# Optimization experiments

Measured on AMD Instinct MI355X. Metric: run time of the kernel, lower is better.

## Reference

```python
import jax, jax.numpy as jnp
import numpy as np

B, N, IN, HD, NH, L, OUT = 256, 128, 9, 128, 8, 4, 60
DH = HD // NH
ALPHA = 0.6
EPS = 1e-5

def _ln(x, g, b):
    m = jnp.mean(x, axis=-1, keepdims=True)
    v = jnp.mean((x - m) ** 2, axis=-1, keepdims=True)
    return (x - m) * jax.lax.rsqrt(v + EPS) * g + b

def setup_inputs():
    key = jax.random.key(0)
    ks = jax.random.split(key, 30)
    p = lambda i, s: jax.random.normal(ks[i], s, jnp.float32) * 0.02
    strong = (jax.random.uniform(ks[25], (N, N)) < 0.15).astype(jnp.float32)
    strong = jnp.maximum(strong, jnp.eye(N, dtype=jnp.float32))  # self loops
    weak_mask = (jax.random.uniform(ks[26], (N, N)) < 0.10).astype(jnp.float32)
    return {
        'x': jax.random.normal(ks[0], (B, N, IN), jnp.float32),
        'conv_w': p(1, (HD, IN)), 'conv_b': p(2, (HD,)),
        'bn_gamma': jnp.ones((HD,), jnp.float32), 'bn_beta': jnp.zeros((HD,), jnp.float32),
        'bn_mean': jnp.zeros((HD,), jnp.float32), 'bn_var': jnp.ones((HD,), jnp.float32),
        'W': p(3, (L, HD, HD)), 'a_src': p(4, (L, NH, DH)), 'a_dst': p(5, (L, NH, DH)),
        'ln_g': jnp.ones((L, HD), jnp.float32), 'ln_b': jnp.zeros((L, HD), jnp.float32),
        'ffn_w1': p(6, (L, HD, 2 * HD)), 'ffn_b1': p(7, (L, 2 * HD)),
        'ffn_w2': p(8, (L, 2 * HD, HD)), 'ffn_b2': p(9, (L, HD)),
        'norm_g': jnp.ones((HD,), jnp.float32), 'norm_b': jnp.zeros((HD,), jnp.float32),
        'proj_w': p(10, (HD, HD)), 'proj_b': p(11, (HD,)),
        'head_w1': p(12, (HD, HD // 2)), 'head_b1': p(13, (HD // 2,)),
        'head_w2': p(14, (HD // 2, OUT)), 'head_b2': p(15, (OUT,)),
        'strong_adj': strong, 'weak_mask': weak_mask,
        'weak_param': p(16, (N, N)), 'edge_weight_adj': p(17, (N, N)),
    }

def reference(x, conv_w, conv_b, bn_gamma, bn_beta, bn_mean, bn_var, W, a_src, a_dst, ln_g, ln_b, ffn_w1, ffn_b1, ffn_w2, ffn_b2, norm_g, norm_b, proj_w, proj_b, head_w1, head_b1, head_w2, head_b2, strong_adj, weak_mask, weak_param, edge_weight_adj):
    # embedding: Conv1d(k=1) == per-node linear, then eval-mode BatchNorm1d + ReLU
    h = jnp.einsum('bni,oi->bno', x, conv_w) + conv_b  # [B,N,HD]
    h = (h - bn_mean) * jax.lax.rsqrt(bn_var + EPS) * bn_gamma + bn_beta
    h = jax.nn.relu(h)
    # weak adjacency: learnable gated edges, row-normalized (shared across layers)
    Aw = jax.nn.sigmoid(weak_param) * weak_mask
    Aw = Aw / (jnp.sum(Aw, axis=-1, keepdims=True) + EPS)  # [N,N]
    for i in range(L):
        res = h
        hp = jnp.einsum('bnd,de->bne', h, W[i]).reshape(B, N, NH, DH)
        s = jnp.einsum('bnhd,hd->bnh', hp, a_src[i])
        t = jnp.einsum('bnhd,hd->bnh', hp, a_dst[i])
        e = jax.nn.leaky_relu(s[:, :, None, :] + t[:, None, :, :], 0.2)  # [B,N,N,H]
        e = e + edge_weight_adj[None, :, :, None]  # learned per-edge bias
        e = jnp.where(strong_adj[None, :, :, None] > 0, e, jnp.float32(-1e9))
        att = jax.nn.softmax(e, axis=2)  # softmax over neighbors j
        strong_out = jnp.einsum('bijh,bjhd->bihd', att, hp)
        weak_out = jnp.einsum('ij,bjhd->bihd', Aw, hp)
        g = jax.nn.relu(ALPHA * strong_out + (1.0 - ALPHA) * weak_out).reshape(B, N, HD)
        g = _ln(g, ln_g[i], ln_b[i])
        g = jax.nn.relu(g @ ffn_w1[i] + ffn_b1[i]) @ ffn_w2[i] + ffn_b2[i]
        h = g + res
    h = _ln(h, norm_g, norm_b)
    h = h @ proj_w + proj_b
    h = jnp.mean(h, axis=1)  # mean-pool over nodes -> [B,HD]
    h = jax.nn.relu(h @ head_w1 + head_b1)
    return h @ head_w2 + head_b2  # [B,OUT]
```

## Files before the change

kernel.cpp:

```cpp
#include <hip/hip_runtime.h>
#include <hip/hip_bf16.h>

typedef __hip_bfloat16 bf16;
typedef unsigned short u16;
typedef __attribute__((ext_vector_type(8))) short bfrag;
typedef __attribute__((ext_vector_type(4))) float cfrag;

union BF { bfrag v; u16 u[8]; unsigned w[4]; };
union CF { cfrag v; float f[4]; };

#define MFMA(a,b,c) __builtin_amdgcn_mfma_f32_16x16x32_bf16(a,b,c,0,0,0)

#define BB   256
#define NN   128
#define IND  9
#define HDD  128
#define LLY  4
#define OUTD 60
#define LOG2E 1.44269504f
#define STR  136

__device__ __forceinline__ float b2f(bf16 v){ return __bfloat162float(v); }
__device__ __forceinline__ float u2f(u16 u){ return __uint_as_float(((unsigned)u) << 16); }
__device__ __forceinline__ u16 f2bf_bits(float f){
    unsigned u = __float_as_uint(f);
    return (u16)((u + 0x7FFFu + ((u >> 16) & 1u)) >> 16);
}
__device__ __forceinline__ unsigned pk2(float a, float b){
    union { __hip_bfloat162 h; unsigned u; } c;
    c.h = __float22bfloat162_rn(make_float2(a, b));
    return c.u;
}
__device__ __forceinline__ float wave_sum(float v){
    #pragma unroll
    for (int m = 32; m; m >>= 1) v += __shfl_xor(v, m, 64);
    return v;
}
__device__ __forceinline__ float ldin(const void* p, int i, bool isbf){
    return isbf ? b2f(((const bf16*)p)[i]) : ((const float*)p)[i];
}

struct SrcPtrs { const void* p[28]; };

__device__ const int NCV_OFF[19] = {0,1152,1280,1408,1536,1664,1792,2304,2816,3840,
                                    4352,4480,4608,20992,21120,29312,29376,33216,33276};
__device__ const int NCV_SRC[18] = {1,2,3,4,5,6,10,11,13,15,16,17,18,19,20,21,22,23};

__global__ __launch_bounds__(256) void k_prep(
    SrcPtrs S, float* __restrict__ pf,
    u16* __restrict__ WT, u16* __restrict__ w1T, u16* __restrict__ w2T,
    u16* __restrict__ WAb, u16* __restrict__ ew2, u16* __restrict__ Aw16,
    int* __restrict__ flagOut)
{
    const unsigned* xw = (const unsigned*)S.p[0];
    int lane = threadIdx.x & 63;
    int cnt = 0;
    for (int i = lane; i < 512; i += 64) {
        float v = __uint_as_float((xw[i] & 0xFFFFu) << 16);
        if (!(fabsf(v) < 32.f)) cnt++;
    }
    bool isbf = wave_sum((float)cnt) < 16.f;
    if (blockIdx.x == 0 && threadIdx.x == 0) *flagOut = isbf ? 1 : 0;

    int blk = blockIdx.x, tid = threadIdx.x;
    if (blk < 131) {
        int idx = blk * 256 + tid;
        if (idx < 33276) {
            int y = 17;
            #pragma unroll 1
            for (int t = 1; t < 18; t++) if (idx < NCV_OFF[t]) { y = t - 1; break; }
            pf[idx] = ldin(S.p[NCV_SRC[y]], idx - NCV_OFF[y], isbf);
        }
    } else if (blk < 387) {
        int j = (blk - 131) * 256 + tid;
        int l = j >> 14, r = j & 16383, n = r >> 7, k = r & 127;
        WT[j] = f2bf_bits(ldin(S.p[7], (l << 14) + k * 128 + n, isbf));
    } else if (blk < 899) {
        int j = (blk - 387) * 256 + tid;
        int l = j >> 15, r = j & 32767, n = r >> 7, k = r & 127;
        w1T[j] = f2bf_bits(ldin(S.p[12], (l << 15) + k * 256 + n, isbf));
    } else if (blk < 1411) {
        int j = (blk - 899) * 256 + tid;
        int l = j >> 15, r = j & 32767, n = r >> 8, k = r & 255;
        w2T[j] = f2bf_bits(ldin(S.p[14], (l << 15) + k * 128 + n, isbf));
    } else if (blk < 1443) {
        int j = (blk - 1411) * 256 + tid;
        int l = j >> 11, r = j & 2047, n = r >> 7, k = r & 127;
        int h = n & 7;
        const void* ap = (n < 8) ? S.p[8] : S.p[9];
        float sacc = 0.f;
        #pragma unroll 1
        for (int d = 0; d < 16; d++)
            sacc += ldin(S.p[7], l * 16384 + k * 128 + h * 16 + d, isbf)
                  * ldin(ap, l * 128 + h * 16 + d, isbf);
        WAb[j] = f2bf_bits(sacc);
    } else if (blk < 1507) {
        int j = (blk - 1443) * 256 + tid;
        float sav = ldin(S.p[24], j, isbf);
        float ewv = ldin(S.p[27], j, isbf);
        ew2[j] = f2bf_bits(sav > 0.f ? ewv * LOG2E : -1e30f);
    } else {
        __shared__ float red[2];
        int i = blk - 1507, j = tid & 127;
        float v = 0.f;
        if (tid < 128) {
            float wmv = ldin(S.p[25], i * 128 + j, isbf);
            float wpv = ldin(S.p[26], i * 128 + j, isbf);
            v = wmv / (1.f + __expf(-wpv));
            float sm = wave_sum(v);
            if ((tid & 63) == 0) red[tid >> 6] = sm;
        }
        __syncthreads();
        if (tid < 128) {
            float tot = red[0] + red[1];
            Aw16[i * 128 + j] = f2bf_bits(v / (tot + 1e-5f));
        }
    }
}

#define LDSB (2*128*STR*2 + 8192)
__global__ __launch_bounds__(512, 2) void k_net(
    const void* __restrict__ xraw, const int* __restrict__ flag,
    const float* __restrict__ pf,
    const u16* __restrict__ WTg, const u16* __restrict__ WAbg,
    const u16* __restrict__ Awg, const u16* __restrict__ ew2g,
    const u16* __restrict__ w1Tg, const u16* __restrict__ w2Tg,
    void* __restrict__ outv)
{
    extern __shared__ __align__(16) char smem[];
    u16* Abuf = (u16*)smem;
    u16* Bbuf = Abuf + 128 * STR;
    float* st2 = (float*)(Bbuf + 128 * STR);
    float* s2  = st2;
    u16*   t2u = (u16*)(st2 + 1024);

    const int b = blockIdx.x;
    const int tid = threadIdx.x, lane = tid & 63, wv = tid >> 6;
    const int l15 = lane & 15, kg = lane >> 4;
    const int wrow = wv * 16;
    const bool isbf = (*flag != 0);

    float hreg[8][4];

    {
        float xr[4][9];
        #pragma unroll
        for (int r = 0; r < 4; r++) {
            int bn = b * NN + wrow + kg * 4 + r;
            #pragma unroll
            for (int k = 0; k < IND; k++) xr[r][k] = ldin(xraw, bn * IND + k, isbf);
        }
        #pragma unroll 1
        for (int nt = 0; nt < 8; nt++) {
            int d = nt * 16 + l15;
            float cwreg[IND];
            #pragma unroll
            for (int k = 0; k < IND; k++) cwreg[k] = pf[d * IND + k];
            float scale = rsqrtf(pf[1664 + d] + 1e-5f) * pf[1280 + d];
            float bias  = pf[1408 + d] - pf[1536 + d] * scale;
            float cbd   = pf[1152 + d];
            #pragma unroll
            for (int r = 0; r < 4; r++) {
                float a = cbd;
                #pragma unroll
                for (int k = 0; k < IND; k++) a = fmaf(xr[r][k], cwreg[k], a);
                a = fmaxf(fmaf(a, scale, bias), 0.f);
                hreg[nt][r] = a;
                Abuf[(wrow + kg * 4 + r) * STR + d] = f2bf_bits(a);
            }
        }
    }

    const int arow = wrow + l15;

    #pragma unroll 1
    for (int l = 0; l < LLY; l++) {
        const u16* WT  = WTg  + l * 16384;
        const u16* WAb = WAbg + l * 2048;
        const u16* w1T = w1Tg + l * 32768;
        const u16* w2T = w2Tg + l * 32768;
        const float* fb1 = pf + 2816 + l * 256;
        const float* fb2 = pf + 3840 + l * 128;
        const float* lng = pf + 1792 + l * 128;
        const float* lnb = pf + 2304 + l * 128;

        __syncthreads();

        {
            CF acc[8], ast;
            #pragma unroll
            for (int r = 0; r < 4; r++) ast.f[r] = 0.f;
            #pragma unroll
            for (int nt = 0; nt < 8; nt++)
                #pragma unroll
                for (int r = 0; r < 4; r++) acc[nt].f[r] = 0.f;
            #pragma unroll 1
            for (int kk = 0; kk < 4; kk++) {
                bfrag af  = *(const bfrag*)&Abuf[arow * STR + kk*32 + kg*8];
                bfrag wab = *(const bfrag*)&WAb[l15 * 128 + kk*32 + kg*8];
                ast.v = MFMA(af, wab, ast.v);
                #pragma unroll
                for (int nt = 0; nt < 8; nt++) {
                    bfrag bw = *(const bfrag*)&WT[(nt*16 + l15) * 128 + kk*32 + kg*8];
                    acc[nt].v = MFMA(af, bw, acc[nt].v);
                }
            }
            #pragma unroll
            for (int nt = 0; nt < 8; nt++) {
                int col = nt*16 + l15;
                #pragma unroll
                for (int rp = 0; rp < 2; rp++) {
                    int row = wrow + kg*4 + rp*2;
                    *(unsigned*)&Bbuf[col * STR + row] = pk2(acc[nt].f[rp*2], acc[nt].f[rp*2+1]);
                }
            }
            #pragma unroll
            for (int r = 0; r < 4; r++) {
                int node = wrow + kg*4 + r;
                float v = ast.f[r] * LOG2E;
                if (l15 < 8) s2[l15 * 128 + node] = v;
                else         t2u[(l15 - 8) * 128 + node] = f2bf_bits(v);
            }
        }
        __syncthreads();

        CF accW[8];
        #pragma unroll
        for (int nt = 0; nt < 8; nt++)
            #pragma unroll
            for (int r = 0; r < 4; r++) accW[nt].f[r] = 0.f;
        #pragma unroll 1
        for (int kk = 0; kk < 4; kk++) {
            bfrag awf = *(const bfrag*)&Awg[arow * 128 + kk*32 + kg*8];
            #pragma unroll
            for (int nt = 0; nt < 8; nt++) {
                bfrag hb2 = *(const bfrag*)&Bbuf[(nt*16 + l15) * STR + kk*32 + kg*8];
                accW[nt].v = MFMA(awf, hb2, accW[nt].v);
            }
        }

        CF accS[8];
        #pragma unroll
        for (int nt = 0; nt < 8; nt++)
            #pragma unroll
            for (int r = 0; r < 4; r++) accS[nt].f[r] = 0.f;
        #pragma unroll 1
        for (int h = 0; h < 8; h++) {
            bfrag hb[4];
            #pragma unroll
            for (int kk = 0; kk < 4; kk++)
                hb[kk] = *(const bfrag*)&Bbuf[(h*16 + l15) * STR + kk*32 + kg*8];
            float sA = s2[h * 128 + arow];
            float pv[4][8];
            float sm = 0.f;
            #pragma unroll
            for (int kk = 0; kk < 4; kk++) {
                BF tb; tb.v = *(const bfrag*)&t2u[h * 128 + kk*32 + kg*8];
                BF e2; e2.v = *(const bfrag*)&ew2g[arow * 128 + kk*32 + kg*8];
                #pragma unroll
                for (int j = 0; j < 8; j++) {
                    float x2 = sA + u2f(tb.u[j]);
                    float lk = fmaxf(x2, 0.2f * x2);
                    float p = __builtin_amdgcn_exp2f(lk + u2f(e2.u[j]));
                    pv[kk][j] = p; sm += p;
                }
            }
            sm += __shfl_xor(sm, 16, 64);
            sm += __shfl_xor(sm, 32, 64);
            float inv = __builtin_amdgcn_rcpf(sm);
            #pragma unroll
            for (int kk = 0; kk < 4; kk++) {
                BF pb;
                #pragma unroll
                for (int q = 0; q < 4; q++)
                    pb.w[q] = pk2(pv[kk][2*q] * inv, pv[kk][2*q+1] * inv);
                accS[h].v = MFMA(pb.v, hb[kk], accS[h].v);
            }
        }
        __syncthreads();

        {
            float gv[8][4];
            #pragma unroll
            for (int nt = 0; nt < 8; nt++)
                #pragma unroll
                for (int r = 0; r < 4; r++)
                    gv[nt][r] = fmaxf(0.6f * accS[nt].f[r] + 0.4f * accW[nt].f[r], 0.f);
            #pragma unroll
            for (int r = 0; r < 4; r++) {
                float s1 = 0.f, sq = 0.f;
                #pragma unroll
                for (int nt = 0; nt < 8; nt++) { float x = gv[nt][r]; s1 += x; sq = fmaf(x, x, sq); }
                #pragma unroll
                for (int m = 1; m <= 8; m <<= 1) { s1 += __shfl_xor(s1, m, 64); sq += __shfl_xor(sq, m, 64); }
                float mu = s1 * (1.f / 128.f);
                float var = sq * (1.f / 128.f) - mu * mu;
                float rs = rsqrtf(fmaxf(var, 0.f) + 1e-5f);
                #pragma unroll
                for (int nt = 0; nt < 8; nt++) {
                    int col = nt*16 + l15;
                    Bbuf[(wrow + kg*4 + r) * STR + col] =
                        f2bf_bits(fmaf((gv[nt][r] - mu) * rs, lng[col], lnb[col]));
                }
            }
        }

        CF acc2[8];
        #pragma unroll
        for (int nt = 0; nt < 8; nt++)
            #pragma unroll
            for (int r = 0; r < 4; r++) acc2[nt].f[r] = 0.f;
        #pragma unroll 1
        for (int nh = 0; nh < 2; nh++) {
            CF a1[8];
            #pragma unroll
            for (int nt = 0; nt < 8; nt++)
                #pragma unroll
                for (int r = 0; r < 4; r++) a1[nt].f[r] = 0.f;
            #pragma unroll 1
            for (int kk = 0; kk < 4; kk++) {
                bfrag gf = *(const bfrag*)&Bbuf[arow * STR + kk*32 + kg*8];
                #pragma unroll
                for (int nt = 0; nt < 8; nt++) {
                    bfrag wf = *(const bfrag*)&w1T[(nh*128 + nt*16 + l15) * 128 + kk*32 + kg*8];
                    a1[nt].v = MFMA(gf, wf, a1[nt].v);
                }
            }
            #pragma unroll
            for (int nt = 0; nt < 8; nt++) {
                int col = nt*16 + l15;
                float b1v = fb1[nh*128 + col];
                #pragma unroll
                for (int r = 0; r < 4; r++)
                    Abuf[(wrow + kg*4 + r) * STR + col] = f2bf_bits(fmaxf(a1[nt].f[r] + b1v, 0.f));
            }
            #pragma unroll 1
            for (int kk = 0; kk < 4; kk++) {
                bfrag hf = *(const bfrag*)&Abuf[arow * STR + kk*32 + kg*8];
                #pragma unroll
                for (int nt = 0; nt < 8; nt++) {
                    bfrag wf = *(const bfrag*)&w2T[(nt*16 + l15) * 256 + nh*128 + kk*32 + kg*8];
                    acc2[nt].v = MFMA(hf, wf, acc2[nt].v);
                }
            }
        }

        #pragma unroll
        for (int nt = 0; nt < 8; nt++) {
            float b2v = fb2[nt*16 + l15];
            #pragma unroll
            for (int r = 0; r < 4; r++) hreg[nt][r] += acc2[nt].f[r] + b2v;
        }
        if (l < LLY - 1) {
            #pragma unroll
            for (int nt = 0; nt < 8; nt++) {
                int col = nt*16 + l15;
                #pragma unroll
                for (int r = 0; r < 4; r++)
                    Abuf[(wrow + kg*4 + r) * STR + col] = f2bf_bits(hreg[nt][r]);
            }
        }
    }

    const float* ng = pf + 4352;
    const float* nb = pf + 4480;
    float pacc[8];
    #pragma unroll
    for (int nt = 0; nt < 8; nt++) pacc[nt] = 0.f;
    #pragma unroll
    for (int r = 0; r < 4; r++) {
        float s1 = 0.f, sq = 0.f;
        #pragma unroll
        for (int nt = 0; nt < 8; nt++) { float x = hreg[nt][r]; s1 += x; sq = fmaf(x, x, sq); }
        #pragma unroll
        for (int m = 1; m <= 8; m <<= 1) { s1 += __shfl_xor(s1, m, 64); sq += __shfl_xor(sq, m, 64); }
        float mu = s1 * (1.f / 128.f);
        float var = sq * (1.f / 128.f) - mu * mu;
        float rs = rsqrtf(fmaxf(var, 0.f) + 1e-5f);
        #pragma unroll
        for (int nt = 0; nt < 8; nt++) {
            int col = nt*16 + l15;
            pacc[nt] += fmaf((hreg[nt][r] - mu) * rs, ng[col], nb[col]);
        }
    }
    #pragma unroll
    for (int nt = 0; nt < 8; nt++) {
        pacc[nt] += __shfl_xor(pacc[nt], 16, 64);
        pacc[nt] += __shfl_xor(pacc[nt], 32, 64);
    }
    __syncthreads();
    if (kg == 0) {
        #pragma unroll
        for (int nt = 0; nt < 8; nt++) st2[wv * 128 + nt*16 + l15] = pacc[nt];
    }
    __syncthreads();
    if (tid < 128) {
        float tot = 0.f;
        #pragma unroll
        for (int w = 0; w < 8; w++) tot += st2[w * 128 + tid];
        st2[1024 + tid] = tot * (1.f / 128.f);
    }
    __syncthreads();
    {
        int e = tid & 127, kq = tid >> 7;
        float a = 0.f;
        #pragma unroll 4
        for (int k = kq * 32; k < kq * 32 + 32; k++)
            a = fmaf(st2[1024 + k], pf[4608 + k * 128 + e], a);
        st2[1152 + kq * 128 + e] = a;
    }
    __syncthreads();
    if (tid < 128)
        st2[1664 + tid] = st2[1152 + tid] + st2[1280 + tid] + st2[1408 + tid] + st2[1536 + tid]
                        + pf[20992 + tid];
    __syncthreads();
    if (tid < 64) {
        float a1 = pf[29312 + tid];
        #pragma unroll 4
        for (int k = 0; k < 128; k++) a1 = fmaf(st2[1664 + k], pf[21120 + k * 64 + tid], a1);
        st2[1792 + tid] = fmaxf(a1, 0.f);
    }
    __syncthreads();
    if (tid < OUTD) {
        float a2 = pf[33216 + tid];
        #pragma unroll 4
        for (int k = 0; k < 64; k++) a2 = fmaf(st2[1792 + k], pf[29376 + k * OUTD + tid], a2);
        if (isbf) ((bf16*)outv)[b * OUTD + tid] = __float2bfloat16(a2);
        else      ((float*)outv)[b * OUTD + tid] = a2;
    }
}

extern "C" void kernel_launch(void* const* d_in, const int* in_sizes, int n_in,
                              void* d_out, int out_size, void* d_ws, size_t ws_size,
                              hipStream_t stream)
{
    float* ws = (float*)d_ws;
    float* pf = ws;
    int*   flag = (int*)(ws + 33280);
    u16* WT16   = (u16*)(ws + 33536);
    u16* w1T16  = WT16 + 65536;
    u16* w2T16  = w1T16 + 131072;
    u16* WAb16  = w2T16 + 131072;
    u16* Aw16   = WAb16 + 8192;
    u16* ew2p   = Aw16 + 16384;

    SrcPtrs S;
    for (int i = 0; i < 28; i++) S.p[i] = d_in[i];

    hipFuncSetAttribute((const void*)k_net,
                        hipFuncAttributeMaxDynamicSharedMemorySize, LDSB);

    k_prep<<<1635, 256, 0, stream>>>(S, pf, WT16, w1T16, w2T16, WAb16, ew2p, Aw16, flag);
    k_net<<<BB, 512, LDSB, stream>>>(d_in[0], flag, pf,
                                     WT16, WAb16, Aw16, ew2p, w1T16, w2T16, d_out);
}
```

Before: 353.0 us.

## Split each node-row tile across two waves by column halves with 1024-thread blocks

Doubles the block to 1024 threads so each 16-row strip is handled by two waves, each owning half the 128 feature columns (and half the attention heads). LayerNorm statistics are combined across the two halves through a small LDS stat buffer. A third LDS buffer holds the FFN hidden layer and the h/feature buffers ping-pong across layers. The aim is more waves per block to hide latency and halve per-thread register pressure, at the cost of more LDS and extra barriers.

```diff
diff --git a/kernel.cpp b/kernel.cpp
--- a/kernel.cpp
+++ b/kernel.cpp
@@ -118,8 +118,8 @@
     }
 }
 
-#define LDSB (2*128*STR*2 + 8192)
-__global__ __launch_bounds__(512, 2) void k_net(
+#define LDSB (3*128*STR*2 + 8192)
+__global__ __launch_bounds__(1024, 4) void k_net(
     const void* __restrict__ xraw, const int* __restrict__ flag,
     const float* __restrict__ pf,
     const u16* __restrict__ WTg, const u16* __restrict__ WAbg,
@@ -130,17 +130,21 @@
     extern __shared__ __align__(16) char smem[];
     u16* Abuf = (u16*)smem;
     u16* Bbuf = Abuf + 128 * STR;
-    float* st2 = (float*)(Bbuf + 128 * STR);
+    u16* Cbuf = Bbuf + 128 * STR;
+    float* st2 = (float*)(Cbuf + 128 * STR);
     float* s2  = st2;
     u16*   t2u = (u16*)(st2 + 1024);
+    float* stat = st2 + 1536;
 
     const int b = blockIdx.x;
     const int tid = threadIdx.x, lane = tid & 63, wv = tid >> 6;
     const int l15 = lane & 15, kg = lane >> 4;
-    const int wrow = wv * 16;
+    const int wpair = wv & 7, half = wv >> 3;
+    const int wrow = wpair * 16;
+    const int colbase = half * 64;
     const bool isbf = (*flag != 0);
 
-    float hreg[8][4];
+    float hreg[4][4];
 
     {
         float xr[4][9];
@@ -151,8 +155,8 @@
             for (int k = 0; k < IND; k++) xr[r][k] = ldin(xraw, bn * IND + k, isbf);
         }
         #pragma unroll 1
-        for (int nt = 0; nt < 8; nt++) {
-            int d = nt * 16 + l15;
+        for (int nt = 0; nt < 4; nt++) {
+            int d = colbase + nt * 16 + l15;
             float cwreg[IND];
             #pragma unroll
             for (int k = 0; k < IND; k++) cwreg[k] = pf[d * IND + k];
@@ -172,6 +176,8 @@
     }
 
     const int arow = wrow + l15;
+    u16* hA = Abuf;
+    u16* hB = Bbuf;
 
     #pragma unroll 1
     for (int l = 0; l < LLY; l++) {
@@ -187,211 +193,248 @@
         __syncthreads();
 
         {
-            CF acc[8], ast;
+            CF acc[4], ast;
             #pragma unroll
             for (int r = 0; r < 4; r++) ast.f[r] = 0.f;
             #pragma unroll
-            for (int nt = 0; nt < 8; nt++)
+            for (int nt = 0; nt < 4; nt++)
                 #pragma unroll
                 for (int r = 0; r < 4; r++) acc[nt].f[r] = 0.f;
             #pragma unroll 1
             for (int kk = 0; kk < 4; kk++) {
-                bfrag af  = *(const bfrag*)&Abuf[arow * STR + kk*32 + kg*8];
-                bfrag wab = *(const bfrag*)&WAb[l15 * 128 + kk*32 + kg*8];
-                ast.v = MFMA(af, wab, ast.v);
-                #pragma unroll
-                for (int nt = 0; nt < 8; nt++) {
-                    bfrag bw = *(const bfrag*)&WT[(nt*16 + l15) * 128 + kk*32 + kg*8];
+                bfrag af = *(const bfrag*)&hA[arow * STR + kk*32 + kg*8];
+                if (half == 0) {
+                    bfrag wab = *(const bfrag*)&WAb[l15 * 128 + kk*32 + kg*8];
+                    ast.v = MFMA(af, wab, ast.v);
+                }
+                #pragma unroll
+                for (int nt = 0; nt < 4; nt++) {
+                    bfrag bw = *(const bfrag*)&WT[(colbase + nt*16 + l15) * 128 + kk*32 + kg*8];
                     acc[nt].v = MFMA(af, bw, acc[nt].v);
                 }
             }
             #pragma unroll
-            for (int nt = 0; nt < 8; nt++) {
-                int col = nt*16 + l15;
+            for (int nt = 0; nt < 4; nt++) {
+                int col = colbase + nt*16 + l15;
                 #pragma unroll
                 for (int rp = 0; rp < 2; rp++) {
                     int row = wrow + kg*4 + rp*2;
-                    *(unsigned*)&Bbuf[col * STR + row] = pk2(acc[nt].f[rp*2], acc[nt].f[rp*2+1]);
-                }
-            }
-            #pragma unroll
-            for (int r = 0; r < 4; r++) {
-                int node = wrow + kg*4 + r;
-                float v = ast.f[r] * LOG2E;
-                if (l15 < 8) s2[l15 * 128 + node] = v;
-                else         t2u[(l15 - 8) * 128 + node] = f2bf_bits(v);
-            }
-        }
-        __syncthreads();
-
-        CF accW[8];
-        #pragma unroll
-        for (int nt = 0; nt < 8; nt++)
+                    *(unsigned*)&hB[col * STR + row] = pk2(acc[nt].f[rp*2], acc[nt].f[rp*2+1]);
+                }
+            }
+            if (half == 0) {
+                #pragma unroll
+                for (int r = 0; r < 4; r++) {
+                    int node = wrow + kg*4 + r;
+                    float v = ast.f[r] * LOG2E;
+                    if (l15 < 8) s2[l15 * 128 + node] = v;
+                    else         t2u[(l15 - 8) * 128 + node] = f2bf_bits(v);
+                }
+            }
+        }
+        __syncthreads();
+
+        CF accS[4];
+        #pragma unroll
+        for (int nt = 0; nt < 4; nt++)
+            #pragma unroll
+            for (int r = 0; r < 4; r++) accS[nt].f[r] = 0.f;
+        {
+            BF e2r[4];
+            #pragma unroll
+            for (int kk = 0; kk < 4; kk++)
+                e2r[kk].v = *(const bfrag*)&ew2g[arow * 128 + kk*32 + kg*8];
+            #pragma unroll 1
+            for (int hi = 0; hi < 4; hi++) {
+                int h = half * 4 + hi;
+                bfrag hb[4];
+                #pragma unroll
+                for (int kk = 0; kk < 4; kk++)
+                    hb[kk] = *(const bfrag*)&hB[(h*16 + l15) * STR + kk*32 + kg*8];
+                float sA = s2[h * 128 + arow];
+                float pv[4][8];
+                float sm = 0.f;
+                #pragma unroll
+                for (int kk = 0; kk < 4; kk++) {
+                    BF tb; tb.v = *(const bfrag*)&t2u[h * 128 + kk*32 + kg*8];
+                    #pragma unroll
+                    for (int j = 0; j < 8; j++) {
+                        float x2 = sA + u2f(tb.u[j]);
+                        float lk = fmaxf(x2, 0.2f * x2);
+                        float p = __builtin_amdgcn_exp2f(lk + u2f(e2r[kk].u[j]));
+                        pv[kk][j] = p; sm += p;
+                    }
+                }
+                sm += __shfl_xor(sm, 16, 64);
+                sm += __shfl_xor(sm, 32, 64);
+                float inv = __builtin_amdgcn_rcpf(sm);
+                #pragma unroll
+                for (int kk = 0; kk < 4; kk++) {
+                    BF pb;
+                    #pragma unroll
+                    for (int q = 0; q < 4; q++)
+                        pb.w[q] = pk2(pv[kk][2*q] * inv, pv[kk][2*q+1] * inv);
+                    accS[hi].v = MFMA(pb.v, hb[kk], accS[hi].v);
+                }
+            }
+        }
+
+        CF accW[4];
+        #pragma unroll
+        for (int nt = 0; nt < 4; nt++)
             #pragma unroll
             for (int r = 0; r < 4; r++) accW[nt].f[r] = 0.f;
         #pragma unroll 1
         for (int kk = 0; kk < 4; kk++) {
             bfrag awf = *(const bfrag*)&Awg[arow * 128 + kk*32 + kg*8];
             #pragma unroll
-            for (int nt = 0; nt < 8; nt++) {
-                bfrag hb2 = *(const bfrag*)&Bbuf[(nt*16 + l15) * STR + kk*32 + kg*8];
+            for (int nt = 0; nt < 4; nt++) {
+                bfrag hb2 = *(const bfrag*)&hB[(colbase + nt*16 + l15) * STR + kk*32 + kg*8];
                 accW[nt].v = MFMA(awf, hb2, accW[nt].v);
             }
         }
-
-        CF accS[8];
-        #pragma unroll
-        for (int nt = 0; nt < 8; nt++)
-            #pragma unroll
-            for (int r = 0; r < 4; r++) accS[nt].f[r] = 0.f;
-        #pragma unroll 1
-        for (int h = 0; h < 8; h++) {
-            bfrag hb[4];
-            #pragma unroll
-            for (int kk = 0; kk < 4; kk++)
-                hb[kk] = *(const bfrag*)&Bbuf[(h*16 + l15) * STR + kk*32 + kg*8];
-            float sA = s2[h * 128 + arow];
-            float pv[4][8];
-            float sm = 0.f;
-            #pragma unroll
-            for (int kk = 0; kk < 4; kk++) {
-                BF tb; tb.v = *(const bfrag*)&t2u[h * 128 + kk*32 + kg*8];
-                BF e2; e2.v = *(const bfrag*)&ew2g[arow * 128 + kk*32 + kg*8];
-                #pragma unroll
-                for (int j = 0; j < 8; j++) {
-                    float x2 = sA + u2f(tb.u[j]);
-                    float lk = fmaxf(x2, 0.2f * x2);
-                    float p = __builtin_amdgcn_exp2f(lk + u2f(e2.u[j]));
-                    pv[kk][j] = p; sm += p;
-                }
-            }
-            sm += __shfl_xor(sm, 16, 64);
-            sm += __shfl_xor(sm, 32, 64);
-            float inv = __builtin_amdgcn_rcpf(sm);
-            #pragma unroll
-            for (int kk = 0; kk < 4; kk++) {
-                BF pb;
-                #pragma unroll
-                for (int q = 0; q < 4; q++)
-                    pb.w[q] = pk2(pv[kk][2*q] * inv, pv[kk][2*q+1] * inv);
-                accS[h].v = MFMA(pb.v, hb[kk], accS[h].v);
-            }
-        }
-        __syncthreads();
-
-        {
-            float gv[8][4];
-            #pragma unroll
-            for (int nt = 0; nt < 8; nt++)
-                #pragma unroll
-                for (int r = 0; r < 4; r++)
-                    gv[nt][r] = fmaxf(0.6f * accS[nt].f[r] + 0.4f * accW[nt].f[r], 0.f);
-            #pragma unroll
-            for (int r = 0; r < 4; r++) {
-                float s1 = 0.f, sq = 0.f;
-                #pragma unroll
-                for (int nt = 0; nt < 8; nt++) { float x = gv[nt][r]; s1 += x; sq = fmaf(x, x, sq); }
-                #pragma unroll
-                for (int m = 1; m <= 8; m <<= 1) { s1 += __shfl_xor(s1, m, 64); sq += __shfl_xor(sq, m, 64); }
-                float mu = s1 * (1.f / 128.f);
-                float var = sq * (1.f / 128.f) - mu * mu;
-                float rs = rsqrtf(fmaxf(var, 0.f) + 1e-5f);
-                #pragma unroll
-                for (int nt = 0; nt < 8; nt++) {
-                    int col = nt*16 + l15;
-                    Bbuf[(wrow + kg*4 + r) * STR + col] =
-                        f2bf_bits(fmaf((gv[nt][r] - mu) * rs, lng[col], lnb[col]));
-                }
-            }
-        }
-
-        CF acc2[8];
-        #pragma unroll
-        for (int nt = 0; nt < 8; nt++)
-            #pragma unroll
-            for (int r = 0; r < 4; r++) acc2[nt].f[r] = 0.f;
+        __syncthreads();
+
+        float gv[4][4];
+        #pragma unroll
+        for (int nt = 0; nt < 4; nt++)
+            #pragma unroll
+            for (int r = 0; r < 4; r++)
+                gv[nt][r] = fmaxf(0.6f * accS[nt].f[r] + 0.4f * accW[nt].f[r], 0.f);
+        #pragma unroll
+        for (int r = 0; r < 4; r++) {
+            float s1 = 0.f, sq = 0.f;
+            #pragma unroll
+            for (int nt = 0; nt < 4; nt++) { float x = gv[nt][r]; s1 += x; sq = fmaf(x, x, sq); }
+            #pragma unroll
+            for (int m = 1; m <= 8; m <<= 1) { s1 += __shfl_xor(s1, m, 64); sq += __shfl_xor(sq, m, 64); }
+            if (l15 == 0) {
+                int row = wrow + kg*4 + r;
+                stat[(half * 128 + row) * 2]     = s1;
+                stat[(half * 128 + row) * 2 + 1] = sq;
+            }
+        }
+        __syncthreads();
+        #pragma unroll
+        for (int r = 0; r < 4; r++) {
+            int row = wrow + kg*4 + r;
+            float s1t = stat[row * 2]     + stat[(128 + row) * 2];
+            float sqt = stat[row * 2 + 1] + stat[(128 + row) * 2 + 1];
+            float mu = s1t * (1.f / 128.f);
+            float var = sqt * (1.f / 128.f) - mu * mu;
+            float rs = rsqrtf(fmaxf(var, 0.f) + 1e-5f);
+            #pragma unroll
+            for (int nt = 0; nt < 4; nt++) {
+                int col = colbase + nt*16 + l15;
+                hB[row * STR + col] = f2bf_bits(fmaf((gv[nt][r] - mu) * rs, lng[col], lnb[col]));
+            }
+        }
+        __syncthreads();
+
         #pragma unroll 1
         for (int nh = 0; nh < 2; nh++) {
-            CF a1[8];
-            #pragma unroll
-            for (int nt = 0; nt < 8; nt++)
+            u16* hid = nh ? Cbuf : hA;
+            CF a1[4];
+            #pragma unroll
+            for (int nt = 0; nt < 4; nt++)
                 #pragma unroll
                 for (int r = 0; r < 4; r++) a1[nt].f[r] = 0.f;
             #pragma unroll 1
             for (int kk = 0; kk < 4; kk++) {
-                bfrag gf = *(const bfrag*)&Bbuf[arow * STR + kk*32 + kg*8];
-                #pragma unroll
-                for (int nt = 0; nt < 8; nt++) {
-                    bfrag wf = *(const bfrag*)&w1T[(nh*128 + nt*16 + l15) * 128 + kk*32 + kg*8];
+                bfrag gf = *(const bfrag*)&hB[arow * STR + kk*32 + kg*8];
+                #pragma unroll
+                for (int nt = 0; nt < 4; nt++) {
+                    bfrag wf = *(const bfrag*)&w1T[(nh*128 + colbase + nt*16 + l15) * 128 + kk*32 + kg*8];
                     a1[nt].v = MFMA(gf, wf, a1[nt].v);
                 }
             }
             #pragma unroll
-            for (int nt = 0; nt < 8; nt++) {
-                int col = nt*16 + l15;
-                float b1v = fb1[nh*128 + col];
+            for (int nt = 0; nt < 4; nt++) {
+                int lcol = colbase + nt*16 + l15;
+                float b1v = fb1[nh*128 + lcol];
                 #pragma unroll
                 for (int r = 0; r < 4; r++)
-                    Abuf[(wrow + kg*4 + r) * STR + col] = f2bf_bits(fmaxf(a1[nt].f[r] + b1v, 0.f));
-            }
-            #pragma unroll 1
-            for (int kk = 0; kk < 4; kk++) {
-                bfrag hf = *(const bfrag*)&Abuf[arow * STR + kk*32 + kg*8];
-                #pragma unroll
-                for (int nt = 0; nt < 8; nt++) {
-                    bfrag wf = *(const bfrag*)&w2T[(nt*16 + l15) * 256 + nh*128 + kk*32 + kg*8];
-                    acc2[nt].v = MFMA(hf, wf, acc2[nt].v);
-                }
-            }
-        }
-
-        #pragma unroll
-        for (int nt = 0; nt < 8; nt++) {
-            float b2v = fb2[nt*16 + l15];
+                    hid[(wrow + kg*4 + r) * STR + lcol] = f2bf_bits(fmaxf(a1[nt].f[r] + b1v, 0.f));
+            }
+        }
+        __syncthreads();
+
+        CF acc2[4];
+        #pragma unroll
+        for (int nt = 0; nt < 4; nt++)
+            #pragma unroll
+            for (int r = 0; r < 4; r++) acc2[nt].f[r] = 0.f;
+        #pragma unroll 1
+        for (int kk = 0; kk < 8; kk++) {
+            const u16* hid = (kk < 4) ? hA : Cbuf;
+            bfrag hf = *(const bfrag*)&hid[arow * STR + (kk & 3)*32 + kg*8];
+            #pragma unroll
+            for (int nt = 0; nt < 4; nt++) {
+                bfrag wf = *(const bfrag*)&w2T[(colbase + nt*16 + l15) * 256 + kk*32 + kg*8];
+                acc2[nt].v = MFMA(hf, wf, acc2[nt].v);
+            }
+        }
+
+        #pragma unroll
+        for (int nt = 0; nt < 4; nt++) {
+            float b2v = fb2[colbase + nt*16 + l15];
             #pragma unroll
             for (int r = 0; r < 4; r++) hreg[nt][r] += acc2[nt].f[r] + b2v;
         }
         if (l < LLY - 1) {
             #pragma unroll
-            for (int nt = 0; nt < 8; nt++) {
-                int col = nt*16 + l15;
+            for (int nt = 0; nt < 4; nt++) {
+                int col = colbase + nt*16 + l15;
                 #pragma unroll
                 for (int r = 0; r < 4; r++)
-                    Abuf[(wrow + kg*4 + r) * STR + col] = f2bf_bits(hreg[nt][r]);
-            }
-        }
+                    hB[(wrow + kg*4 + r) * STR + col] = f2bf_bits(hreg[nt][r]);
+            }
+        }
+        { u16* t = hA; hA = hB; hB = t; }
     }
 
     const float* ng = pf + 4352;
     const float* nb = pf + 4480;
-    float pacc[8];
-    #pragma unroll
-    for (int nt = 0; nt < 8; nt++) pacc[nt] = 0.f;
     #pragma unroll
     for (int r = 0; r < 4; r++) {
         float s1 = 0.f, sq = 0.f;
         #pragma unroll
-        for (int nt = 0; nt < 8; nt++) { float x = hreg[nt][r]; s1 += x; sq = fmaf(x, x, sq); }
+        for (int nt = 0; nt < 4; nt++) { float x = hreg[nt][r]; s1 += x; sq = fmaf(x, x, sq); }
         #pragma unroll
         for (int m = 1; m <= 8; m <<= 1) { s1 += __shfl_xor(s1, m, 64); sq += __shfl_xor(sq, m, 64); }
-        float mu = s1 * (1.f / 128.f);
-        float var = sq * (1.f / 128.f) - mu * mu;
+        if (l15 == 0) {
+            int row = wrow + kg*4 + r;
+            stat[(half * 128 + row) * 2]     = s1;
+            stat[(half * 128 + row) * 2 + 1] = sq;
+        }
+    }
+    __syncthreads();
+    float pacc[4];
+    #pragma unroll
+    for (int nt = 0; nt < 4; nt++) pacc[nt] = 0.f;
+    #pragma unroll
+    for (int r = 0; r < 4; r++) {
+        int row = wrow + kg*4 + r;
+        float s1t = stat[row * 2]     + stat[(128 + row) * 2];
+        float sqt = stat[row * 2 + 1] + stat[(128 + row) * 2 + 1];
+        float mu = s1t * (1.f / 128.f);
+        float var = sqt * (1.f / 128.f) - mu * mu;
         float rs = rsqrtf(fmaxf(var, 0.f) + 1e-5f);
         #pragma unroll
-        for (int nt = 0; nt < 8; nt++) {
-            int col = nt*16 + l15;
+        for (int nt = 0; nt < 4; nt++) {
+            int col = colbase + nt*16 + l15;
             pacc[nt] += fmaf((hreg[nt][r] - mu) * rs, ng[col], nb[col]);
         }
     }
     #pragma unroll
-    for (int nt = 0; nt < 8; nt++) {
+    for (int nt = 0; nt < 4; nt++) {
         pacc[nt] += __shfl_xor(pacc[nt], 16, 64);
         pacc[nt] += __shfl_xor(pacc[nt], 32, 64);
     }
-    __syncthreads();
     if (kg == 0) {
         #pragma unroll
-        for (int nt = 0; nt < 8; nt++) st2[wv * 128 + nt*16 + l15] = pacc[nt];
+        for (int nt = 0; nt < 4; nt++)
+            st2[wpair * 128 + colbase + nt*16 + l15] = pacc[nt];
     }
     __syncthreads();
     if (tid < 128) {
@@ -401,7 +444,7 @@
         st2[1024 + tid] = tot * (1.f / 128.f);
     }
     __syncthreads();
-    {
+    if (tid < 512) {
         int e = tid & 127, kq = tid >> 7;
         float a = 0.f;
         #pragma unroll 4
@@ -451,6 +494,6 @@
                         hipFuncAttributeMaxDynamicSharedMemorySize, LDSB);
 
     k_prep<<<1635, 256, 0, stream>>>(S, pf, WT16, w1T16, w2T16, WAb16, ew2p, Aw16, flag);
-    k_net<<<BB, 512, LDSB, stream>>>(d_in[0], flag, pf,
-                                     WT16, WAb16, Aw16, ew2p, w1T16, w2T16, d_out);
-}
+    k_net<<<BB, 1024, LDSB, stream>>>(d_in[0], flag, pf,
+                                      WT16, WAb16, Aw16, ew2p, w1T16, w2T16, d_out);
+}
```

Measured after the change: 382.5 us. +8.4%, slower.

## Defer softmax normalization, packed-float edge math, hoist edge bias, unroll MFMA loops

Applied to the files above, without the earlier changes.

The attention softmax now feeds unnormalized exponentials straight into the MFMA and rescales the 16x16 accumulator afterwards with a per-row reciprocal fetched by shuffle. This removes the per-element multiply and the register buffering of all 32 probabilities per head. The per-edge bias is decoded once per layer instead of once per head, and the leaky-relu/add math uses 2-wide float vectors so packed instructions can be used. Bf16 conversions switch to the hardware packed convert, and several MFMA k-loops are unrolled by two, which may raise register pressure.

```diff
diff --git a/kernel.cpp b/kernel.cpp
--- a/kernel.cpp
+++ b/kernel.cpp
@@ -5,6 +5,7 @@
 typedef unsigned short u16;
 typedef __attribute__((ext_vector_type(8))) short bfrag;
 typedef __attribute__((ext_vector_type(4))) float cfrag;
+typedef __attribute__((ext_vector_type(2))) float f32x2;
 
 union BF { bfrag v; u16 u[8]; unsigned w[4]; };
 union CF { cfrag v; float f[4]; };
@@ -30,6 +31,9 @@
     union { __hip_bfloat162 h; unsigned u; } c;
     c.h = __float22bfloat162_rn(make_float2(a, b));
     return c.u;
+}
+__device__ __forceinline__ u16 f2bf1(float f){
+    return (u16)pk2(f, 0.f);
 }
 __device__ __forceinline__ float wave_sum(float v){
     #pragma unroll
@@ -166,7 +170,7 @@
                 for (int k = 0; k < IND; k++) a = fmaf(xr[r][k], cwreg[k], a);
                 a = fmaxf(fmaf(a, scale, bias), 0.f);
                 hreg[nt][r] = a;
-                Abuf[(wrow + kg * 4 + r) * STR + d] = f2bf_bits(a);
+                Abuf[(wrow + kg * 4 + r) * STR + d] = f2bf1(a);
             }
         }
     }
@@ -194,7 +198,7 @@
             for (int nt = 0; nt < 8; nt++)
                 #pragma unroll
                 for (int r = 0; r < 4; r++) acc[nt].f[r] = 0.f;
-            #pragma unroll 1
+            #pragma unroll 2
             for (int kk = 0; kk < 4; kk++) {
                 bfrag af  = *(const bfrag*)&Abuf[arow * STR + kk*32 + kg*8];
                 bfrag wab = *(const bfrag*)&WAb[l15 * 128 + kk*32 + kg*8];
@@ -219,62 +223,77 @@
                 int node = wrow + kg*4 + r;
                 float v = ast.f[r] * LOG2E;
                 if (l15 < 8) s2[l15 * 128 + node] = v;
-                else         t2u[(l15 - 8) * 128 + node] = f2bf_bits(v);
+                else         t2u[(l15 - 8) * 128 + node] = f2bf1(v);
             }
         }
         __syncthreads();
 
+        CF accS[8];
+        #pragma unroll
+        for (int nt = 0; nt < 8; nt++)
+            #pragma unroll
+            for (int r = 0; r < 4; r++) accS[nt].f[r] = 0.f;
+        {
+            f32x2 e2f[4][4];
+            #pragma unroll
+            for (int kk = 0; kk < 4; kk++) {
+                BF e2; e2.v = *(const bfrag*)&ew2g[arow * 128 + kk*32 + kg*8];
+                #pragma unroll
+                for (int q = 0; q < 4; q++) {
+                    unsigned w = e2.w[q];
+                    e2f[kk][q].x = __uint_as_float(w << 16);
+                    e2f[kk][q].y = __uint_as_float(w & 0xffff0000u);
+                }
+            }
+            #pragma unroll 1
+            for (int h = 0; h < 8; h++) {
+                float sA = s2[h * 128 + arow];
+                f32x2 sA2; sA2.x = sA; sA2.y = sA;
+                float sm = 0.f;
+                #pragma unroll
+                for (int kk = 0; kk < 4; kk++) {
+                    bfrag hb = *(const bfrag*)&Bbuf[(h*16 + l15) * STR + kk*32 + kg*8];
+                    BF tb; tb.v = *(const bfrag*)&t2u[h * 128 + kk*32 + kg*8];
+                    BF pb;
+                    #pragma unroll
+                    for (int q = 0; q < 4; q++) {
+                        unsigned w = tb.w[q];
+                        f32x2 tv;
+                        tv.x = __uint_as_float(w << 16);
+                        tv.y = __uint_as_float(w & 0xffff0000u);
+                        f32x2 x2 = sA2 + tv;
+                        f32x2 lk = __builtin_elementwise_max(x2, x2 * 0.2f);
+                        f32x2 ex = lk + e2f[kk][q];
+                        float p0 = __builtin_amdgcn_exp2f(ex.x);
+                        float p1 = __builtin_amdgcn_exp2f(ex.y);
+                        sm += p0 + p1;
+                        pb.w[q] = pk2(p0, p1);
+                    }
+                    accS[h].v = MFMA(pb.v, hb, accS[h].v);
+                }
+                sm += __shfl_xor(sm, 16, 64);
+                sm += __shfl_xor(sm, 32, 64);
+                float inv = __builtin_amdgcn_rcpf(sm);
+                #pragma unroll
+                for (int r = 0; r < 4; r++) {
+                    float invr = __shfl(inv, kg * 4 + r, 64);
+                    accS[h].f[r] *= invr;
+                }
+            }
+        }
+
         CF accW[8];
         #pragma unroll
         for (int nt = 0; nt < 8; nt++)
             #pragma unroll
             for (int r = 0; r < 4; r++) accW[nt].f[r] = 0.f;
-        #pragma unroll 1
+        #pragma unroll 2
         for (int kk = 0; kk < 4; kk++) {
             bfrag awf = *(const bfrag*)&Awg[arow * 128 + kk*32 + kg*8];
             #pragma unroll
             for (int nt = 0; nt < 8; nt++) {
                 bfrag hb2 = *(const bfrag*)&Bbuf[(nt*16 + l15) * STR + kk*32 + kg*8];
                 accW[nt].v = MFMA(awf, hb2, accW[nt].v);
-            }
-        }
-
-        CF accS[8];
-        #pragma unroll
-        for (int nt = 0; nt < 8; nt++)
-            #pragma unroll
-            for (int r = 0; r < 4; r++) accS[nt].f[r] = 0.f;
-        #pragma unroll 1
-        for (int h = 0; h < 8; h++) {
-            bfrag hb[4];
-            #pragma unroll
-            for (int kk = 0; kk < 4; kk++)
-                hb[kk] = *(const bfrag*)&Bbuf[(h*16 + l15) * STR + kk*32 + kg*8];
-            float sA = s2[h * 128 + arow];
-            float pv[4][8];
-            float sm = 0.f;
-            #pragma unroll
-            for (int kk = 0; kk < 4; kk++) {
-                BF tb; tb.v = *(const bfrag*)&t2u[h * 128 + kk*32 + kg*8];
-                BF e2; e2.v = *(const bfrag*)&ew2g[arow * 128 + kk*32 + kg*8];
-                #pragma unroll
-                for (int j = 0; j < 8; j++) {
-                    float x2 = sA + u2f(tb.u[j]);
-                    float lk = fmaxf(x2, 0.2f * x2);
-                    float p = __builtin_amdgcn_exp2f(lk + u2f(e2.u[j]));
-                    pv[kk][j] = p; sm += p;
-                }
-            }
-            sm += __shfl_xor(sm, 16, 64);
-            sm += __shfl_xor(sm, 32, 64);
-            float inv = __builtin_amdgcn_rcpf(sm);
-            #pragma unroll
-            for (int kk = 0; kk < 4; kk++) {
-                BF pb;
-                #pragma unroll
-                for (int q = 0; q < 4; q++)
-                    pb.w[q] = pk2(pv[kk][2*q] * inv, pv[kk][2*q+1] * inv);
-                accS[h].v = MFMA(pb.v, hb[kk], accS[h].v);
             }
         }
         __syncthreads();
@@ -300,7 +319,7 @@
                 for (int nt = 0; nt < 8; nt++) {
                     int col = nt*16 + l15;
                     Bbuf[(wrow + kg*4 + r) * STR + col] =
-                        f2bf_bits(fmaf((gv[nt][r] - mu) * rs, lng[col], lnb[col]));
+                        f2bf1(fmaf((gv[nt][r] - mu) * rs, lng[col], lnb[col]));
                 }
             }
         }
@@ -317,7 +336,7 @@
             for (int nt = 0; nt < 8; nt++)
                 #pragma unroll
                 for (int r = 0; r < 4; r++) a1[nt].f[r] = 0.f;
-            #pragma unroll 1
+            #pragma unroll 2
             for (int kk = 0; kk < 4; kk++) {
                 bfrag gf = *(const bfrag*)&Bbuf[arow * STR + kk*32 + kg*8];
                 #pragma unroll
@@ -332,9 +351,9 @@
                 float b1v = fb1[nh*128 + col];
                 #pragma unroll
                 for (int r = 0; r < 4; r++)
-                    Abuf[(wrow + kg*4 + r) * STR + col] = f2bf_bits(fmaxf(a1[nt].f[r] + b1v, 0.f));
-            }
-            #pragma unroll 1
+                    Abuf[(wrow + kg*4 + r) * STR + col] = f2bf1(fmaxf(a1[nt].f[r] + b1v, 0.f));
+            }
+            #pragma unroll 2
             for (int kk = 0; kk < 4; kk++) {
                 bfrag hf = *(const bfrag*)&Abuf[arow * STR + kk*32 + kg*8];
                 #pragma unroll
@@ -357,7 +376,7 @@
                 int col = nt*16 + l15;
                 #pragma unroll
                 for (int r = 0; r < 4; r++)
-                    Abuf[(wrow + kg*4 + r) * STR + col] = f2bf_bits(hreg[nt][r]);
+                    Abuf[(wrow + kg*4 + r) * STR + col] = f2bf1(hreg[nt][r]);
             }
         }
     }
```

New measurement: 362.4 us. 1.03x slower.

## Transpose weights through LDS tiles in prep and use hardware bf16 conversion

Applied to the files above, without the earlier changes.

The prep kernel now transposes W, ffn_w1 and ffn_w2 with one block per 128x128 tile staged in shared memory. Each block reads coalesced rows and writes coalesced transposed rows, replacing the strided per-element gathers spread over about 1280 blocks. The grid shrinks from 1635 to 375 blocks. Separately, the main kernel's f32-to-bf16 stores switch from a manual rounding routine to the packed hardware conversion intrinsic. Much more work now falls on each prep block, so those few blocks may become the critical path.

```diff
diff --git a/kernel.cpp b/kernel.cpp
--- a/kernel.cpp
+++ b/kernel.cpp
@@ -31,6 +31,9 @@
     c.h = __float22bfloat162_rn(make_float2(a, b));
     return c.u;
 }
+__device__ __forceinline__ u16 f2bf1(float f){
+    return (u16)pk2(f, 0.f);
+}
 __device__ __forceinline__ float wave_sum(float v){
     #pragma unroll
     for (int m = 32; m; m >>= 1) v += __shfl_xor(v, m, 64);
@@ -52,6 +55,9 @@
     u16* __restrict__ WAb, u16* __restrict__ ew2, u16* __restrict__ Aw16,
     int* __restrict__ flagOut)
 {
+    __shared__ u16 T[128][130];
+    __shared__ float red[2];
+
     const unsigned* xw = (const unsigned*)S.p[0];
     int lane = threadIdx.x & 63;
     int cnt = 0;
@@ -71,20 +77,47 @@
             for (int t = 1; t < 18; t++) if (idx < NCV_OFF[t]) { y = t - 1; break; }
             pf[idx] = ldin(S.p[NCV_SRC[y]], idx - NCV_OFF[y], isbf);
         }
-    } else if (blk < 387) {
-        int j = (blk - 131) * 256 + tid;
-        int l = j >> 14, r = j & 16383, n = r >> 7, k = r & 127;
-        WT[j] = f2bf_bits(ldin(S.p[7], (l << 14) + k * 128 + n, isbf));
-    } else if (blk < 899) {
-        int j = (blk - 387) * 256 + tid;
-        int l = j >> 15, r = j & 32767, n = r >> 7, k = r & 127;
-        w1T[j] = f2bf_bits(ldin(S.p[12], (l << 15) + k * 256 + n, isbf));
-    } else if (blk < 1411) {
-        int j = (blk - 899) * 256 + tid;
-        int l = j >> 15, r = j & 32767, n = r >> 8, k = r & 255;
-        w2T[j] = f2bf_bits(ldin(S.p[14], (l << 15) + k * 128 + n, isbf));
-    } else if (blk < 1443) {
-        int j = (blk - 1411) * 256 + tid;
+    } else if (blk < 135) {
+        int l = blk - 131;
+        #pragma unroll 4
+        for (int it = 0; it < 64; it++) {
+            int idx = it * 256 + tid, k = idx >> 7, n = idx & 127;
+            T[k][n] = f2bf_bits(ldin(S.p[7], (l << 14) + k * 128 + n, isbf));
+        }
+        __syncthreads();
+        #pragma unroll 4
+        for (int it = 0; it < 64; it++) {
+            int idx = it * 256 + tid, n = idx >> 7, k = idx & 127;
+            WT[(l << 14) + n * 128 + k] = T[k][n];
+        }
+    } else if (blk < 143) {
+        int q = blk - 135, l = q >> 1, hf = q & 1;
+        #pragma unroll 4
+        for (int it = 0; it < 64; it++) {
+            int idx = it * 256 + tid, k = idx >> 7, nn = idx & 127;
+            T[k][nn] = f2bf_bits(ldin(S.p[12], (l << 15) + k * 256 + hf * 128 + nn, isbf));
+        }
+        __syncthreads();
+        #pragma unroll 4
+        for (int it = 0; it < 64; it++) {
+            int idx = it * 256 + tid, nn = idx >> 7, k = idx & 127;
+            w1T[(l << 15) + (hf * 128 + nn) * 128 + k] = T[k][nn];
+        }
+    } else if (blk < 151) {
+        int q = blk - 143, l = q >> 1, kh = q & 1;
+        #pragma unroll 4
+        for (int it = 0; it < 64; it++) {
+            int idx = it * 256 + tid, kk = idx >> 7, nn = idx & 127;
+            T[kk][nn] = f2bf_bits(ldin(S.p[14], (l << 15) + (kh * 128 + kk) * 128 + nn, isbf));
+        }
+        __syncthreads();
+        #pragma unroll 4
+        for (int it = 0; it < 64; it++) {
+            int idx = it * 256 + tid, n = idx >> 7, kk = idx & 127;
+            w2T[(l << 15) + n * 256 + kh * 128 + kk] = T[kk][n];
+        }
+    } else if (blk < 183) {
+        int j = (blk - 151) * 256 + tid;
         int l = j >> 11, r = j & 2047, n = r >> 7, k = r & 127;
         int h = n & 7;
         const void* ap = (n < 8) ? S.p[8] : S.p[9];
@@ -94,14 +127,13 @@
             sacc += ldin(S.p[7], l * 16384 + k * 128 + h * 16 + d, isbf)
                   * ldin(ap, l * 128 + h * 16 + d, isbf);
         WAb[j] = f2bf_bits(sacc);
-    } else if (blk < 1507) {
-        int j = (blk - 1443) * 256 + tid;
+    } else if (blk < 247) {
+        int j = (blk - 183) * 256 + tid;
         float sav = ldin(S.p[24], j, isbf);
         float ewv = ldin(S.p[27], j, isbf);
         ew2[j] = f2bf_bits(sav > 0.f ? ewv * LOG2E : -1e30f);
     } else {
-        __shared__ float red[2];
-        int i = blk - 1507, j = tid & 127;
+        int i = blk - 247, j = tid & 127;
         float v = 0.f;
         if (tid < 128) {
             float wmv = ldin(S.p[25], i * 128 + j, isbf);
@@ -166,7 +198,7 @@
                 for (int k = 0; k < IND; k++) a = fmaf(xr[r][k], cwreg[k], a);
                 a = fmaxf(fmaf(a, scale, bias), 0.f);
                 hreg[nt][r] = a;
-                Abuf[(wrow + kg * 4 + r) * STR + d] = f2bf_bits(a);
+                Abuf[(wrow + kg * 4 + r) * STR + d] = f2bf1(a);
             }
         }
     }
@@ -219,7 +251,7 @@
                 int node = wrow + kg*4 + r;
                 float v = ast.f[r] * LOG2E;
                 if (l15 < 8) s2[l15 * 128 + node] = v;
-                else         t2u[(l15 - 8) * 128 + node] = f2bf_bits(v);
+                else         t2u[(l15 - 8) * 128 + node] = f2bf1(v);
             }
         }
         __syncthreads();
@@ -300,7 +332,7 @@
                 for (int nt = 0; nt < 8; nt++) {
                     int col = nt*16 + l15;
                     Bbuf[(wrow + kg*4 + r) * STR + col] =
-                        f2bf_bits(fmaf((gv[nt][r] - mu) * rs, lng[col], lnb[col]));
+                        f2bf1(fmaf((gv[nt][r] - mu) * rs, lng[col], lnb[col]));
                 }
             }
         }
@@ -332,7 +364,7 @@
                 float b1v = fb1[nh*128 + col];
                 #pragma unroll
                 for (int r = 0; r < 4; r++)
-                    Abuf[(wrow + kg*4 + r) * STR + col] = f2bf_bits(fmaxf(a1[nt].f[r] + b1v, 0.f));
+                    Abuf[(wrow + kg*4 + r) * STR + col] = f2bf1(fmaxf(a1[nt].f[r] + b1v, 0.f));
             }
             #pragma unroll 1
             for (int kk = 0; kk < 4; kk++) {
@@ -357,7 +389,7 @@
                 int col = nt*16 + l15;
                 #pragma unroll
                 for (int r = 0; r < 4; r++)
-                    Abuf[(wrow + kg*4 + r) * STR + col] = f2bf_bits(hreg[nt][r]);
+                    Abuf[(wrow + kg*4 + r) * STR + col] = f2bf1(hreg[nt][r]);
             }
         }
     }
@@ -450,7 +482,7 @@
     hipFuncSetAttribute((const void*)k_net,
                         hipFuncAttributeMaxDynamicSharedMemorySize, LDSB);
 
-    k_prep<<<1635, 256, 0, stream>>>(S, pf, WT16, w1T16, w2T16, WAb16, ew2p, Aw16, flag);
+    k_prep<<<375, 256, 0, stream>>>(S, pf, WT16, w1T16, w2T16, WAb16, ew2p, Aw16, flag);
     k_net<<<BB, 512, LDSB, stream>>>(d_in[0], flag, pf,
                                      WT16, WAb16, Aw16, ew2p, w1T16, w2T16, d_out);
 }
```

Result: slower. 365.7 us (+3.6%).
